# Kernel tuning notes

Measured on AMD Instinct MI355X. Metric: run time of the kernel, lower is better.

Reference implementation:

```python
import jax, jax.numpy as jnp
import numpy as np

B, L, S, N, D, DT, V, H = 32, 256, 5, 1024, 256, 256, 512, 8
Dh = D // H


def layernorm(x, g, b, eps=1e-5):
    m = x.mean(-1, keepdims=True)
    v = ((x - m) ** 2).mean(-1, keepdims=True)
    return (x - m) / jnp.sqrt(v + eps) * g + b


def setup_inputs() -> dict:
    key = jax.random.key(0)
    ks = jax.random.split(key, 16)
    sc = lambda k, shape: jax.random.normal(k, shape, jnp.float32) * 0.02
    return {
        'vis_tokens': jax.random.normal(ks[0], (B, N, D), jnp.float32),
        'left_ctx_ids': jax.random.randint(ks[1], (B, L, S), 0, V),
        'right_ctx_ids': jax.random.randint(ks[2], (B, L, S), 0, V),
        'tgt_ids': jax.random.randint(ks[3], (B, L), 0, V),
        'tgt_mask': jnp.ones((B, L), jnp.float32),
        'vis_mask': jax.random.uniform(ks[4], (B, L, N), jnp.float32),
        'emb_w': sc(ks[5], (V, DT)),          # tied embedding / classifier weight
        'dir_left': sc(ks[6], (DT,)),
        'dir_right': sc(ks[7], (DT,)),
        'txt_proj_w': sc(ks[8], (D, DT)), 'txt_proj_b': jnp.zeros((D,), jnp.float32),
        'q_gamma': jnp.ones((D,), jnp.float32), 'q_beta': jnp.zeros((D,), jnp.float32),
        'k_w': sc(ks[9], (D, D)), 'k_b': jnp.zeros((D,), jnp.float32),
        'v_w': sc(ks[10], (D, D)), 'v_b': jnp.zeros((D,), jnp.float32),
        'kv_gamma': jnp.ones((D,), jnp.float32), 'kv_beta': jnp.zeros((D,), jnp.float32),
        'tau': jnp.asarray(1.0, jnp.float32),
        'cls_b': jnp.zeros((V,), jnp.float32),
        'conv_w_l': sc(ks[11], (DT, DT, 3)),   # fresh random conv weight per call in torch
        'conv_w_r': sc(ks[12], (DT, DT, 3)),
    }


def _ctx_to_query(ctx_ids, dir_tok, conv_w, emb_w, txt_proj_w, txt_proj_b, qg, qb):
    E = emb_w[ctx_ids]                                    # [B,L,S,DT]
    q = jnp.transpose(E, (0, 1, 3, 2)).reshape(B * L, DT, S)
    q = jax.lax.conv_general_dilated(q, conv_w, (1,), [(1, 1)],
                                     dimension_numbers=('NCH', 'OIH', 'NCH'))  # [B*L,DT,S]
    # faithful to torch: flat reinterpretation [B*L,DT,S] -> [B,L,S,DT], then mean over dim 2
    q = q.reshape(B, L, -1, DT).mean(2)                   # [B,L,DT]
    q = q + dir_tok
    return layernorm(q @ txt_proj_w.T + txt_proj_b, qg, qb)  # [B,L,D]


def _cross_attend(Q, Fv, vis_mask, k_w, k_b, v_w, v_b, kvg, kvb, tau):
    K = layernorm(Fv @ k_w.T + k_b, kvg, kvb)             # [B,N,D]
    Vv = layernorm(Fv @ v_w.T + v_b, kvg, kvb)
    q = Q.reshape(B, L, H, Dh).transpose(0, 2, 1, 3)      # [B,H,L,Dh]
    k = K.reshape(B, N, H, Dh).transpose(0, 2, 1, 3)
    v = Vv.reshape(B, N, H, Dh).transpose(0, 2, 1, 3)
    tau_c = jnp.clip(tau, 0.25, 4.0)
    scores = jnp.einsum('bhld,bhnd->bhln', q, k) / (Dh ** 0.5 * tau_c)
    scores = scores * vis_mask[:, None]                   # multiplicative mask
    attn = jax.nn.softmax(scores, axis=-1)                # dropout = identity (eval)
    out = jnp.einsum('bhln,bhnd->bhld', attn, v)
    return out.transpose(0, 2, 1, 3).reshape(B, L, D)


def reference(vis_tokens, left_ctx_ids, right_ctx_ids, tgt_ids, tgt_mask, vis_mask,
              emb_w, dir_left, dir_right, txt_proj_w, txt_proj_b, q_gamma, q_beta,
              k_w, k_b, v_w, v_b, kv_gamma, kv_beta, tau, cls_b, conv_w_l, conv_w_r):
    Ql = _ctx_to_query(left_ctx_ids, dir_left, conv_w_l, emb_w, txt_proj_w, txt_proj_b, q_gamma, q_beta)
    Qr = _ctx_to_query(right_ctx_ids, dir_right, conv_w_r, emb_w, txt_proj_w, txt_proj_b, q_gamma, q_beta)
    Fl = _cross_attend(Ql, vis_tokens, vis_mask, k_w, k_b, v_w, v_b, kv_gamma, kv_beta, tau)
    Fr = _cross_attend(Qr, vis_tokens, vis_mask, k_w, k_b, v_w, v_b, kv_gamma, kv_beta, tau)
    logits_l = Fl @ emb_w.T + cls_b                       # tied classifier
    logits_r = Fr @ emb_w.T + cls_b
    p_l = jax.nn.softmax(logits_l / 2.0, axis=-1)
    p_r = jax.nn.softmax(logits_r / 2.0, axis=-1)
    agree = ((p_l[:, :-1, :] - p_r[:, 1:, :]) ** 2).sum(-1)
    denom = jnp.maximum(tgt_mask[:, :-1].sum(), 1.0)
    loss_sgm = 0.1 * (agree * tgt_mask[:, :-1]).sum() / denom
    return loss_sgm, logits_l, logits_r
```

## Files before the change

kernel.cpp:

```cpp
#include <hip/hip_runtime.h>

typedef __attribute__((ext_vector_type(8))) short short8;
typedef __attribute__((ext_vector_type(4))) short short4v;
typedef __attribute__((ext_vector_type(4))) float f32x4;

__device__ __forceinline__ short f2bf(float x) {
    union { float f; unsigned u; } c; c.f = x;
    unsigned u = c.u;
    u += 0x7fffu + ((u >> 16) & 1u);
    return (short)(u >> 16);
}

__global__ __launch_bounds__(256) void cvt_bf16(const float* __restrict__ s, short* __restrict__ d, int n4) {
    int i = blockIdx.x * 256 + threadIdx.x;
    if (i < n4) {
        float4 v = ((const float4*)s)[i];
        short4 o;
        o.x = f2bf(v.x); o.y = f2bf(v.y); o.z = f2bf(v.z); o.w = f2bf(v.w);
        ((short4*)d)[i] = o;
    }
}

__global__ __launch_bounds__(256) void cvt3(const float* __restrict__ emb, const float* __restrict__ kw,
                                            const float* __restrict__ vw,
                                            short* __restrict__ de, short* __restrict__ dk, short* __restrict__ dv) {
    int i = blockIdx.x * 256 + threadIdx.x;
    const float* s; short* d; int off;
    if (i < 32768) { s = emb; d = de; off = i; }
    else if (i < 49152) { s = kw; d = dk; off = i - 32768; }
    else { s = vw; d = dv; off = i - 49152; }
    float4 v = ((const float4*)s)[off];
    short4 o;
    o.x = f2bf(v.x); o.y = f2bf(v.y); o.z = f2bf(v.z); o.w = f2bf(v.w);
    ((short4*)d)[off] = o;
}

__global__ void build_wfold(const float* __restrict__ cl, const float* __restrict__ cr,
                            float* __restrict__ wfT) {
    const float* conv_w = blockIdx.y ? cr : cl;
    float* o = wfT + (long)blockIdx.y * 327680;
    const int j = blockIdx.x;
    const int ci = threadIdx.x;
    float acc[5] = {0.f, 0.f, 0.f, 0.f, 0.f};
#pragma unroll
    for (int i = 0; i < 5; ++i) {
        int flat = i * 256 + j;
        int c = flat / 5;
        int s = flat % 5;
#pragma unroll
        for (int k = 0; k < 3; ++k) {
            int si = s + k - 1;
            if (si >= 0 && si < 5) acc[si] += conv_w[(c * 256 + ci) * 3 + k];
        }
    }
#pragma unroll
    for (int si = 0; si < 5; ++si)
        o[(si * 256 + ci) * 256 + j] = acc[si] * 0.2f;
}

template <bool BIAS>
__global__ __launch_bounds__(256) void gemm64(const float* __restrict__ A,
                                              const float* __restrict__ W,
                                              const float* __restrict__ bias,
                                              float* __restrict__ C,
                                              int K, int ldC,
                                              long sliceA, long sliceW, long sliceC) {
    A += (long)blockIdx.z * sliceA;
    W += (long)blockIdx.z * sliceW;
    C += (long)blockIdx.z * sliceC;
    const int row0 = blockIdx.x * 64;
    const int col0 = blockIdx.y * 64;
    __shared__ float As[32][68];
    __shared__ float Ws[32][68];
    const int t = threadIdx.x;
    const int tx = t & 15;
    const int ty = t >> 4;
    float acc[4][4] = {};
    for (int kk = 0; kk < K; kk += 32) {
#pragma unroll
        for (int e = 0; e < 8; ++e) {
            int f = t + 256 * e;
            int r = f >> 5, kc = f & 31;
            As[kc][r] = A[(long)(row0 + r) * K + kk + kc];
            Ws[kc][r] = W[(long)(col0 + r) * K + kk + kc];
        }
        __syncthreads();
#pragma unroll
        for (int kc = 0; kc < 32; ++kc) {
            float4 a4 = *(const float4*)&As[kc][ty * 4];
            float4 w4 = *(const float4*)&Ws[kc][tx * 4];
            float av[4] = {a4.x, a4.y, a4.z, a4.w};
            float wv[4] = {w4.x, w4.y, w4.z, w4.w};
#pragma unroll
            for (int i = 0; i < 4; ++i)
#pragma unroll
                for (int jj = 0; jj < 4; ++jj)
                    acc[i][jj] += av[i] * wv[jj];
        }
        __syncthreads();
    }
#pragma unroll
    for (int r = 0; r < 4; ++r) {
        int row = row0 + ty * 4 + r;
#pragma unroll
        for (int c = 0; c < 4; ++c) {
            int col = col0 + tx * 4 + c;
            float v = acc[r][c];
            if (BIAS) v += bias[col];
            C[(long)row * ldC + col] = v;
        }
    }
}

__global__ __launch_bounds__(256) void gemm_bf(const short* __restrict__ A,
                                               const short* __restrict__ W,
                                               const float* __restrict__ bias,
                                               float* __restrict__ Cf,
                                               int K, int ldC,
                                               long sliceA, long sliceC) {
    A += (long)blockIdx.z * sliceA;
    const int row0 = blockIdx.x * 64, col0 = blockIdx.y * 64;
    __shared__ short As[64 * 40];
    __shared__ short Ws[64 * 40];
    const int t = threadIdx.x;
    const int wid = t >> 6, lane = t & 63, sub = lane & 15, quad = lane >> 4;
    const int wy = wid >> 1, wx = wid & 1;
    const int srow = t >> 2, sseg = t & 3;
    f32x4 acc00 = {0.f, 0.f, 0.f, 0.f}, acc01 = acc00, acc10 = acc00, acc11 = acc00;
    for (int kk = 0; kk < K; kk += 32) {
        *(short8*)&As[srow * 40 + sseg * 8] = *(const short8*)&A[(long)(row0 + srow) * K + kk + sseg * 8];
        *(short8*)&Ws[srow * 40 + sseg * 8] = *(const short8*)&W[(long)(col0 + srow) * K + kk + sseg * 8];
        __syncthreads();
        short8 a0 = *(const short8*)&As[(wy * 32 + sub) * 40 + quad * 8];
        short8 a1 = *(const short8*)&As[(wy * 32 + 16 + sub) * 40 + quad * 8];
        short8 b0 = *(const short8*)&Ws[(wx * 32 + sub) * 40 + quad * 8];
        short8 b1 = *(const short8*)&Ws[(wx * 32 + 16 + sub) * 40 + quad * 8];
        acc00 = __builtin_amdgcn_mfma_f32_16x16x32_bf16(a0, b0, acc00, 0, 0, 0);
        acc01 = __builtin_amdgcn_mfma_f32_16x16x32_bf16(a0, b1, acc01, 0, 0, 0);
        acc10 = __builtin_amdgcn_mfma_f32_16x16x32_bf16(a1, b0, acc10, 0, 0, 0);
        acc11 = __builtin_amdgcn_mfma_f32_16x16x32_bf16(a1, b1, acc11, 0, 0, 0);
        __syncthreads();
    }
    Cf += (long)blockIdx.z * sliceC;
#pragma unroll
    for (int i = 0; i < 2; ++i)
#pragma unroll
        for (int j = 0; j < 2; ++j) {
            f32x4 a = (i == 0) ? (j == 0 ? acc00 : acc01) : (j == 0 ? acc10 : acc11);
#pragma unroll
            for (int r = 0; r < 4; ++r) {
                int row = row0 + wy * 32 + i * 16 + quad * 4 + r;
                int col = col0 + wx * 32 + j * 16 + sub;
                Cf[(long)row * ldC + col] = a[r] + bias[col];
            }
        }
}

__global__ __launch_bounds__(256) void gemm_ln(const short* __restrict__ A,
                                               const short* __restrict__ kwbf, const short* __restrict__ vwbf,
                                               const float* __restrict__ k_b, const float* __restrict__ v_b,
                                               const float* __restrict__ gamma, const float* __restrict__ beta,
                                               short* __restrict__ Kout, short* __restrict__ Vt) {
    const bool isV = blockIdx.y != 0;
    const short* W = isV ? vwbf : kwbf;
    const float* bias = isV ? v_b : k_b;
    const int row0 = blockIdx.x * 64;
    __shared__ short As[64 * 40];
    __shared__ short Ws[256 * 40];
    __shared__ float s_mu[64 * 4];
    __shared__ float s_sq[64 * 4];
    __shared__ float s_mv[64 * 2];
    const int t = threadIdx.x;
    const int wid = t >> 6, lane = t & 63, sub = lane & 15, quad = lane >> 4;
    f32x4 acc[4][4];
#pragma unroll
    for (int mi = 0; mi < 4; ++mi)
#pragma unroll
        for (int ni = 0; ni < 4; ++ni) acc[mi][ni] = (f32x4){0.f, 0.f, 0.f, 0.f};

    const int sr = t >> 2, sseg = t & 3;
    for (int kk = 0; kk < 256; kk += 32) {
        *(short8*)&As[sr * 40 + sseg * 8] = *(const short8*)&A[(long)(row0 + sr) * 256 + kk + sseg * 8];
#pragma unroll
        for (int i = 0; i < 4; ++i) {
            int r = i * 64 + sr;
            *(short8*)&Ws[r * 40 + sseg * 8] = *(const short8*)&W[(long)r * 256 + kk + sseg * 8];
        }
        __syncthreads();
        short8 a[4], b[4];
#pragma unroll
        for (int mi = 0; mi < 4; ++mi) a[mi] = *(const short8*)&As[(mi * 16 + sub) * 40 + quad * 8];
#pragma unroll
        for (int ni = 0; ni < 4; ++ni) b[ni] = *(const short8*)&Ws[(wid * 64 + ni * 16 + sub) * 40 + quad * 8];
#pragma unroll
        for (int mi = 0; mi < 4; ++mi)
#pragma unroll
            for (int ni = 0; ni < 4; ++ni)
                acc[mi][ni] = __builtin_amdgcn_mfma_f32_16x16x32_bf16(a[mi], b[ni], acc[mi][ni], 0, 0, 0);
        __syncthreads();
    }
#pragma unroll
    for (int ni = 0; ni < 4; ++ni) {
        float bv = bias[wid * 64 + ni * 16 + sub];
#pragma unroll
        for (int mi = 0; mi < 4; ++mi)
#pragma unroll
            for (int r = 0; r < 4; ++r) acc[mi][ni][r] += bv;
    }
#pragma unroll
    for (int mi = 0; mi < 4; ++mi) {
#pragma unroll
        for (int r = 0; r < 4; ++r) {
            float s = 0.f, q2 = 0.f;
#pragma unroll
            for (int ni = 0; ni < 4; ++ni) {
                float v = acc[mi][ni][r];
                s += v; q2 += v * v;
            }
#pragma unroll
            for (int off = 8; off; off >>= 1) {
                s += __shfl_xor(s, off, 16);
                q2 += __shfl_xor(q2, off, 16);
            }
            if (sub == 0) {
                int row = mi * 16 + quad * 4 + r;
                s_mu[row * 4 + wid] = s;
                s_sq[row * 4 + wid] = q2;
            }
        }
    }
    __syncthreads();
    if (t < 64) {
        float s = s_mu[t * 4] + s_mu[t * 4 + 1] + s_mu[t * 4 + 2] + s_mu[t * 4 + 3];
        float q2 = s_sq[t * 4] + s_sq[t * 4 + 1] + s_sq[t * 4 + 2] + s_sq[t * 4 + 3];
        float mean = s * (1.0f / 256.0f);
        float var = q2 * (1.0f / 256.0f) - mean * mean;
        s_mv[t * 2] = mean;
        s_mv[t * 2 + 1] = rsqrtf(var + 1e-5f);
    }
    __syncthreads();
#pragma unroll
    for (int ni = 0; ni < 4; ++ni) {
        int col = wid * 64 + ni * 16 + sub;
        float g = gamma[col], bb = beta[col];
        if (!isV) {
#pragma unroll
            for (int mi = 0; mi < 4; ++mi)
#pragma unroll
                for (int r = 0; r < 4; ++r) {
                    int row = mi * 16 + quad * 4 + r;
                    float v = (acc[mi][ni][r] - s_mv[row * 2]) * s_mv[row * 2 + 1] * g + bb;
                    Kout[(long)(row0 + row) * 256 + col] = f2bf(v);
                }
        } else {
            int h = col >> 5, dh = col & 31;
#pragma unroll
            for (int mi = 0; mi < 4; ++mi) {
                int rowb = row0 + mi * 16 + quad * 4;
                short4 o;
#pragma unroll
                for (int r = 0; r < 4; ++r) {
                    int row = mi * 16 + quad * 4 + r;
                    float v = (acc[mi][ni][r] - s_mv[row * 2]) * s_mv[row * 2 + 1] * g + bb;
                    ((short*)&o)[r] = f2bf(v);
                }
                int gb = rowb >> 10, n = rowb & 1023;
                *(short4*)&Vt[((long)(gb * 8 + h) * 32 + dh) * 1024 + n] = o;
            }
        }
    }
}

__global__ void bias_dir_kernel(const float* __restrict__ tp, const float* __restrict__ tpb,
                                const float* __restrict__ dirL, const float* __restrict__ dirR,
                                float* __restrict__ biasL, float* __restrict__ biasR) {
    const float* dir = blockIdx.x ? dirR : dirL;
    float* outp = blockIdx.x ? biasR : biasL;
    __shared__ float sdir[256];
    const int d = threadIdx.x;
    sdir[d] = dir[d];
    __syncthreads();
    float acc = tpb[d];
    for (int j = 0; j < 256; ++j) acc += tp[d * 256 + j] * sdir[j];
    outp[d] = acc;
}

__global__ __launch_bounds__(256) void q_build(const int* __restrict__ idsL, const int* __restrict__ idsR,
                                               const float* __restrict__ Pp,
                                               const float* __restrict__ biasL, const float* __restrict__ biasR,
                                               const float* __restrict__ qg, const float* __restrict__ qb,
                                               short* __restrict__ Qbf) {
    const int wid = threadIdx.x >> 6, lane = threadIdx.x & 63;
    const int bl = blockIdx.x * 4 + wid;
    const bool right = blockIdx.y != 0;
    const int* ids = right ? idsR : idsL;
    const float* P = right ? Pp + 655360 : Pp;
    const float* bias = right ? biasR : biasL;
    const int d0 = lane * 4;
    float4 acc = *(const float4*)&bias[d0];
#pragma unroll
    for (int s = 0; s < 5; ++s) {
        int tok = ids[bl * 5 + s];
        float4 p = *(const float4*)&P[(long)(s * 512 + tok) * 256 + d0];
        acc.x += p.x; acc.y += p.y; acc.z += p.z; acc.w += p.w;
    }
    float sum = acc.x + acc.y + acc.z + acc.w;
    float sq = acc.x * acc.x + acc.y * acc.y + acc.z * acc.z + acc.w * acc.w;
#pragma unroll
    for (int off = 32; off; off >>= 1) {
        sum += __shfl_xor(sum, off, 64);
        sq += __shfl_xor(sq, off, 64);
    }
    float mean = sum * (1.0f / 256.0f);
    float var = sq * (1.0f / 256.0f) - mean * mean;
    float rstd = rsqrtf(var + 1e-5f);
    float4 g = *(const float4*)&qg[d0];
    float4 bb = *(const float4*)&qb[d0];
    short4 o;
    o.x = f2bf((acc.x - mean) * rstd * g.x + bb.x);
    o.y = f2bf((acc.y - mean) * rstd * g.y + bb.y);
    o.z = f2bf((acc.z - mean) * rstd * g.z + bb.z);
    o.w = f2bf((acc.w - mean) * rstd * g.w + bb.w);
    *(short4*)&Qbf[(right ? 2097152L : 0L) + (long)bl * 256 + d0] = o;
}

__device__ __forceinline__ void proc_chunk(
    short8 ak0, short8 ak1, short4v v00, short4v v01, short4v v10, short4v v11,
    const float* mlds, int sub, int quad, float inv2,
    const short8 (&bqL)[4], const short8 (&bqR)[4],
    f32x4 (&oL)[4][2], f32x4 (&oR)[4][2], float (&psL)[4], float (&psR)[4]) {
    short8 av0, av1;
#pragma unroll
    for (int j = 0; j < 4; ++j) {
        av0[j] = v00[j]; av0[4 + j] = v01[j];
        av1[j] = v10[j]; av1[4 + j] = v11[j];
    }
    const int sw = (quad ^ (sub & 7)) << 2;
#pragma unroll
    for (int lt = 0; lt < 4; ++lt) {
        const int mi = ((lt * 16 + sub) << 5) + sw;
        float4 mk0 = *(const float4*)&mlds[mi];
        float4 mk1 = *(const float4*)&mlds[mi ^ 16];
        float m0x = mk0.x * inv2, m0y = mk0.y * inv2, m0z = mk0.z * inv2, m0w = mk0.w * inv2;
        float m1x = mk1.x * inv2, m1y = mk1.y * inv2, m1z = mk1.z * inv2, m1w = mk1.w * inv2;
        {
            f32x4 c0 = {0.f, 0.f, 0.f, 0.f}, c1 = c0;
            c0 = __builtin_amdgcn_mfma_f32_16x16x32_bf16(ak0, bqL[lt], c0, 0, 0, 0);
            c1 = __builtin_amdgcn_mfma_f32_16x16x32_bf16(ak1, bqL[lt], c1, 0, 0, 0);
            float p0 = __builtin_amdgcn_exp2f(c0[0] * m0x);
            float p1 = __builtin_amdgcn_exp2f(c0[1] * m0y);
            float p2 = __builtin_amdgcn_exp2f(c0[2] * m0z);
            float p3 = __builtin_amdgcn_exp2f(c0[3] * m0w);
            float p4 = __builtin_amdgcn_exp2f(c1[0] * m1x);
            float p5 = __builtin_amdgcn_exp2f(c1[1] * m1y);
            float p6 = __builtin_amdgcn_exp2f(c1[2] * m1z);
            float p7 = __builtin_amdgcn_exp2f(c1[3] * m1w);
            psL[lt] += ((p0 + p1) + (p2 + p3)) + ((p4 + p5) + (p6 + p7));
            short8 p8;
            p8[0] = f2bf(p0); p8[1] = f2bf(p1); p8[2] = f2bf(p2); p8[3] = f2bf(p3);
            p8[4] = f2bf(p4); p8[5] = f2bf(p5); p8[6] = f2bf(p6); p8[7] = f2bf(p7);
            oL[lt][0] = __builtin_amdgcn_mfma_f32_16x16x32_bf16(av0, p8, oL[lt][0], 0, 0, 0);
            oL[lt][1] = __builtin_amdgcn_mfma_f32_16x16x32_bf16(av1, p8, oL[lt][1], 0, 0, 0);
        }
        {
            f32x4 c0 = {0.f, 0.f, 0.f, 0.f}, c1 = c0;
            c0 = __builtin_amdgcn_mfma_f32_16x16x32_bf16(ak0, bqR[lt], c0, 0, 0, 0);
            c1 = __builtin_amdgcn_mfma_f32_16x16x32_bf16(ak1, bqR[lt], c1, 0, 0, 0);
            float p0 = __builtin_amdgcn_exp2f(c0[0] * m0x);
            float p1 = __builtin_amdgcn_exp2f(c0[1] * m0y);
            float p2 = __builtin_amdgcn_exp2f(c0[2] * m0z);
            float p3 = __builtin_amdgcn_exp2f(c0[3] * m0w);
            float p4 = __builtin_amdgcn_exp2f(c1[0] * m1x);
            float p5 = __builtin_amdgcn_exp2f(c1[1] * m1y);
            float p6 = __builtin_amdgcn_exp2f(c1[2] * m1z);
            float p7 = __builtin_amdgcn_exp2f(c1[3] * m1w);
            psR[lt] += ((p0 + p1) + (p2 + p3)) + ((p4 + p5) + (p6 + p7));
            short8 p8;
            p8[0] = f2bf(p0); p8[1] = f2bf(p1); p8[2] = f2bf(p2); p8[3] = f2bf(p3);
            p8[4] = f2bf(p4); p8[5] = f2bf(p5); p8[6] = f2bf(p6); p8[7] = f2bf(p7);
            oR[lt][0] = __builtin_amdgcn_mfma_f32_16x16x32_bf16(av0, p8, oR[lt][0], 0, 0, 0);
            oR[lt][1] = __builtin_amdgcn_mfma_f32_16x16x32_bf16(av1, p8, oR[lt][1], 0, 0, 0);
        }
    }
}

__global__ __launch_bounds__(512, 1) void attn_wave(const short* __restrict__ Qbf,
                                                    const short* __restrict__ Kbf,
                                                    const short* __restrict__ Vt,
                                                    const float* __restrict__ vis_mask,
                                                    const float* __restrict__ tau_p,
                                                    short* __restrict__ Fbf) {
    const int t = threadIdx.x;
    const int wid = t >> 6, lane = t & 63, sub = lane & 15, quad = lane >> 4;
    const int gb = ((blockIdx.x & 7) << 5) | (blockIdx.x >> 3);
    const int b = gb >> 3;
    const int lb = (gb >> 1) & 3;
    const int hq = gb & 1;
    const int wh = wid >> 1, nh = wid & 1;
    const int h = hq * 4 + wh;
    const int l0 = lb * 64;
    float tau = fminf(fmaxf(tau_p[0], 0.25f), 4.0f);
    const float inv2 = 1.4426950408889634f / (5.656854249492381f * tau);

    __shared__ float mbuf[2 * 4096];
    __shared__ float red[4][64][72];

    const int s0 = t * 2;
    const int l_s = (s0 >> 3) & 63, nh_s = s0 >> 9;
    const int n4a = s0 & 7, n4b = n4a + 1;
    const float* mrow0 = vis_mask + (long)(b * 256 + l0 + l_s) * 1024 + nh_s * 512 + 4 * (n4a ^ (l_s & 7));
    const float* mrow1 = vis_mask + (long)(b * 256 + l0 + l_s) * 1024 + nh_s * 512 + 4 * (n4b ^ (l_s & 7));
    float* mdst0 = mbuf + nh_s * 2048 + l_s * 32 + n4a * 4;
    float* mdst1 = mbuf + nh_s * 2048 + l_s * 32 + n4b * 4;

    short8 bqL[4], bqR[4];
#pragma unroll
    for (int lt = 0; lt < 4; ++lt) {
        const long qoff = (long)(b * 256 + l0 + lt * 16 + sub) * 256 + h * 32 + quad * 8;
        bqL[lt] = *(const short8*)&Qbf[qoff];
        bqR[lt] = *(const short8*)&Qbf[2097152 + qoff];
    }

    const short* Kb = Kbf + (long)b * 262144 + h * 32;
    const short* Vb = Vt + (long)(b * 8 + h) * 32768;
    const float* mld = mbuf + nh * 2048;

    f32x4 oL[4][2], oR[4][2];
    float psL[4], psR[4];
#pragma unroll
    for (int lt = 0; lt < 4; ++lt) {
        oL[lt][0] = (f32x4){0.f, 0.f, 0.f, 0.f}; oL[lt][1] = oL[lt][0];
        oR[lt][0] = oL[lt][0]; oR[lt][1] = oL[lt][0];
        psL[lt] = 0.f; psR[lt] = 0.f;
    }

    const int nbeg = nh << 9;

#define LOADK(A0, A1, N)                                                      \
    A0 = *(const short8*)&Kb[(long)((N) + sub) * 256 + quad * 8];             \
    A1 = *(const short8*)&Kb[(long)((N) + 16 + sub) * 256 + quad * 8];
#define LOADV(W00, W01, W10, W11, N)                                          \
    W00 = *(const short4v*)&Vb[(long)sub * 1024 + (N) + quad * 4];            \
    W01 = *(const short4v*)&Vb[(long)sub * 1024 + (N) + 16 + quad * 4];       \
    W10 = *(const short4v*)&Vb[(long)(16 + sub) * 1024 + (N) + quad * 4];     \
    W11 = *(const short4v*)&Vb[(long)(16 + sub) * 1024 + (N) + 16 + quad * 4];

    short8 ak0A, ak1A, ak0B, ak1B;
    short4v v00A, v01A, v10A, v11A, v00B, v01B, v10B, v11B;
    float4 mr0, mr1;

    mr0 = *(const float4*)&mrow0[0];
    mr1 = *(const float4*)&mrow1[0];
    *(float4*)&mdst0[0] = mr0;
    *(float4*)&mdst1[0] = mr1;
    LOADK(ak0A, ak1A, nbeg)
    LOADV(v00A, v01A, v10A, v11A, nbeg)
    __syncthreads();

#pragma unroll 1
    for (int j = 0; j < 8; ++j) {
        const int n0 = nbeg + j * 64;
        LOADK(ak0B, ak1B, n0 + 32)
        LOADV(v00B, v01B, v10B, v11B, n0 + 32)
        {
            const int nrel = j * 64 + 32;
            mr0 = *(const float4*)&mrow0[nrel];
            mr1 = *(const float4*)&mrow1[nrel];
        }
        proc_chunk(ak0A, ak1A, v00A, v01A, v10A, v11A, mld, sub, quad, inv2,
                   bqL, bqR, oL, oR, psL, psR);
        *(float4*)&mdst0[4096] = mr0;
        *(float4*)&mdst1[4096] = mr1;
        __syncthreads();
        const int nx = (j < 7) ? n0 + 64 : nbeg;
        LOADK(ak0A, ak1A, nx)
        LOADV(v00A, v01A, v10A, v11A, nx)
        {
            const int nrel = (j < 7) ? j * 64 + 64 : 0;
            mr0 = *(const float4*)&mrow0[nrel];
            mr1 = *(const float4*)&mrow1[nrel];
        }
        proc_chunk(ak0B, ak1B, v00B, v01B, v10B, v11B, mld + 4096, sub, quad, inv2,
                   bqL, bqR, oL, oR, psL, psR);
        *(float4*)&mdst0[0] = mr0;
        *(float4*)&mdst1[0] = mr1;
        __syncthreads();
    }
#undef LOADK
#undef LOADV

#pragma unroll
    for (int lt = 0; lt < 4; ++lt) {
        psL[lt] += __shfl_xor(psL[lt], 16, 64); psL[lt] += __shfl_xor(psL[lt], 32, 64);
        psR[lt] += __shfl_xor(psR[lt], 16, 64); psR[lt] += __shfl_xor(psR[lt], 32, 64);
    }

    if (nh == 1) {
        float* p = &red[wh][lane][0];
#pragma unroll
        for (int lt = 0; lt < 4; ++lt) {
            *(f32x4*)(p + lt * 8) = oL[lt][0];
            *(f32x4*)(p + lt * 8 + 4) = oL[lt][1];
            *(f32x4*)(p + 32 + lt * 8) = oR[lt][0];
            *(f32x4*)(p + 32 + lt * 8 + 4) = oR[lt][1];
            p[64 + lt] = psL[lt];
            p[68 + lt] = psR[lt];
        }
    }
    __syncthreads();
    if (nh == 1) return;
    {
        const float* p = &red[wh][lane][0];
#pragma unroll
        for (int lt = 0; lt < 4; ++lt) {
            f32x4 e0 = *(const f32x4*)(p + lt * 8);
            f32x4 e1 = *(const f32x4*)(p + lt * 8 + 4);
            f32x4 e2 = *(const f32x4*)(p + 32 + lt * 8);
            f32x4 e3 = *(const f32x4*)(p + 32 + lt * 8 + 4);
#pragma unroll
            for (int r = 0; r < 4; ++r) {
                oL[lt][0][r] += e0[r]; oL[lt][1][r] += e1[r];
                oR[lt][0][r] += e2[r]; oR[lt][1][r] += e3[r];
            }
            psL[lt] += p[64 + lt];
            psR[lt] += p[68 + lt];
        }
    }

#pragma unroll
    for (int lt = 0; lt < 4; ++lt) {
        const long fo = (long)(b * 256 + l0 + lt * 16 + sub) * 256 + h * 32 + quad * 4;
        const float rL = 1.0f / psL[lt], rR = 1.0f / psR[lt];
        short4v s0v, s1v;
#pragma unroll
        for (int r = 0; r < 4; ++r) { s0v[r] = f2bf(oL[lt][0][r] * rL); s1v[r] = f2bf(oL[lt][1][r] * rL); }
        *(short4v*)&Fbf[fo] = s0v;
        *(short4v*)&Fbf[fo + 16] = s1v;
#pragma unroll
        for (int r = 0; r < 4; ++r) { s0v[r] = f2bf(oR[lt][0][r] * rR); s1v[r] = f2bf(oR[lt][1][r] * rR); }
        *(short4v*)&Fbf[2097152 + fo] = s0v;
        *(short4v*)&Fbf[2097152 + fo + 16] = s1v;
    }
}

__global__ __launch_bounds__(256) void loss_pair(const float* __restrict__ logits,
                                                 const float* __restrict__ tgt_mask,
                                                 float* __restrict__ partials) {
    const int wid = threadIdx.x >> 6, lane = threadIdx.x & 63;
    const int pid = blockIdx.x * 4 + wid;
    const int b = pid / 255, l = pid - b * 255;
    const float* ll = logits + (long)(b * 256 + l) * 512;
    const float* lr = logits + 4194304 + (long)(b * 256 + l + 1) * 512;
    float a[8], c[8];
#pragma unroll
    for (int j = 0; j < 8; ++j) {
        a[j] = ll[lane + 64 * j] * 0.5f;
        c[j] = lr[lane + 64 * j] * 0.5f;
    }
    float ml = -1e30f, mr = -1e30f;
#pragma unroll
    for (int j = 0; j < 8; ++j) { ml = fmaxf(ml, a[j]); mr = fmaxf(mr, c[j]); }
#pragma unroll
    for (int off = 32; off; off >>= 1) {
        ml = fmaxf(ml, __shfl_xor(ml, off, 64));
        mr = fmaxf(mr, __shfl_xor(mr, off, 64));
    }
    float sl = 0.f, sr = 0.f;
#pragma unroll
    for (int j = 0; j < 8; ++j) {
        a[j] = __expf(a[j] - ml); sl += a[j];
        c[j] = __expf(c[j] - mr); sr += c[j];
    }
#pragma unroll
    for (int off = 32; off; off >>= 1) {
        sl += __shfl_xor(sl, off, 64);
        sr += __shfl_xor(sr, off, 64);
    }
    float rl = 1.0f / sl, rr = 1.0f / sr;
    float sq = 0.f;
#pragma unroll
    for (int j = 0; j < 8; ++j) {
        float d = a[j] * rl - c[j] * rr;
        sq += d * d;
    }
#pragma unroll
    for (int off = 32; off; off >>= 1) sq += __shfl_xor(sq, off, 64);

    __shared__ float sred[4];
    if (lane == 0) sred[wid] = sq * tgt_mask[b * 256 + l];
    __syncthreads();
    if (threadIdx.x == 0)
        partials[blockIdx.x] = (sred[0] + sred[1]) + (sred[2] + sred[3]);
}

__global__ __launch_bounds__(256) void loss_final(const float* __restrict__ tgt_mask,
                                                  const float* __restrict__ partials,
                                                  float* __restrict__ outp) {
    const int t = threadIdx.x;
    float s = 0.f, acc = 0.f;
    for (int i = t; i < 32 * 255; i += 256) {
        int b = i / 255, l = i % 255;
        s += tgt_mask[b * 256 + l];
    }
    for (int i = t; i < 2040; i += 256) acc += partials[i];
    __shared__ float red[256];
    __shared__ float reda[256];
    red[t] = s;
    reda[t] = acc;
    __syncthreads();
    for (int st = 128; st; st >>= 1) {
        if (t < st) { red[t] += red[t + st]; reda[t] += reda[t + st]; }
        __syncthreads();
    }
    if (t == 0) outp[0] = 0.1f * reda[0] / fmaxf(red[0], 1.0f);
}

extern "C" void kernel_launch(void* const* d_in, const int* in_sizes, int n_in,
                              void* d_out, int out_size, void* d_ws, size_t ws_size,
                              hipStream_t stream) {
    const float* vis_tokens = (const float*)d_in[0];
    const int* idsL = (const int*)d_in[1];
    const int* idsR = (const int*)d_in[2];
    const float* tgt_mask = (const float*)d_in[4];
    const float* vis_mask = (const float*)d_in[5];
    const float* emb_w = (const float*)d_in[6];
    const float* dirL = (const float*)d_in[7];
    const float* dirR = (const float*)d_in[8];
    const float* tp_w = (const float*)d_in[9];
    const float* tp_b = (const float*)d_in[10];
    const float* q_g = (const float*)d_in[11];
    const float* q_b = (const float*)d_in[12];
    const float* k_w = (const float*)d_in[13];
    const float* k_b = (const float*)d_in[14];
    const float* v_w = (const float*)d_in[15];
    const float* v_b = (const float*)d_in[16];
    const float* kv_g = (const float*)d_in[17];
    const float* kv_b = (const float*)d_in[18];
    const float* tau = (const float*)d_in[19];
    const float* cls_b = (const float*)d_in[20];
    const float* conv_l = (const float*)d_in[21];
    const float* conv_r = (const float*)d_in[22];
    float* out = (float*)d_out;

    short* sws = (short*)d_ws;
    short* visbf = sws;
    short* embbf = visbf + 8388608;
    short* kwbf  = embbf + 131072;
    short* vwbf  = kwbf + 65536;
    short* Kbf   = vwbf + 65536;
    short* Vt    = Kbf + 8388608;
    short* Qbf   = Vt + 8388608;
    short* Fbf   = Qbf + 4194304;
    float* wfT   = (float*)(Fbf + 4194304);
    float* Ms    = wfT + 655360;
    float* Pp    = Ms + 655360;
    float* bias_l = Pp + 1310720;
    float* bias_r = bias_l + 256;
    float* partials = bias_r + 256;

    cvt_bf16<<<8192, 256, 0, stream>>>(vis_tokens, visbf, 2097152);
    cvt3<<<256, 256, 0, stream>>>(emb_w, k_w, v_w, embbf, kwbf, vwbf);

    build_wfold<<<dim3(256, 2), 256, 0, stream>>>(conv_l, conv_r, wfT);
    gemm64<false><<<dim3(4, 4, 10), 256, 0, stream>>>(tp_w, wfT, nullptr, Ms, 256, 256, 0, 65536, 65536);
    gemm64<false><<<dim3(8, 4, 10), 256, 0, stream>>>(emb_w, Ms, nullptr, Pp, 256, 256, 0, 65536, 131072);
    bias_dir_kernel<<<2, 256, 0, stream>>>(tp_w, tp_b, dirL, dirR, bias_l, bias_r);
    q_build<<<dim3(2048, 2), 256, 0, stream>>>(idsL, idsR, Pp, bias_l, bias_r, q_g, q_b, Qbf);

    gemm_ln<<<dim3(512, 2), 256, 0, stream>>>(visbf, kwbf, vwbf, k_b, v_b, kv_g, kv_b, Kbf, Vt);

    attn_wave<<<256, 512, 0, stream>>>(Qbf, Kbf, Vt, vis_mask, tau, Fbf);

    gemm_bf<<<dim3(128, 8, 2), 256, 0, stream>>>(Fbf, embbf, cls_b, out + 1, 256, 512,
                                                 2097152, 4194304);

    loss_pair<<<2040, 256, 0, stream>>>(out + 1, tgt_mask, partials);
    loss_final<<<1, 256, 0, stream>>>(tgt_mask, partials, out);
}
```

Before: 334.5 us.

## Split attention key range across four waves per head with 1024-thread blocks

The attention kernel doubles its block to 1024 threads, so each head's 1024 visual tokens are split across four waves instead of two. Each wave now runs four loop iterations instead of eight, and the per-wave partial results are combined in three serialized shared-memory reduction rounds. Other changes: the mask is pre-scaled by the softmax constant when staged into LDS, the bf16 conversion uses packed hardware intrinsics, and K/V are loaded just before use rather than software-prefetched a chunk ahead. The intent is more waves per CU to hide latency. The costs are extra reduction rounds and barriers, and load latency is no longer hidden by the explicit prefetch.

```diff
diff --git a/kernel.cpp b/kernel.cpp
--- a/kernel.cpp
+++ b/kernel.cpp
@@ -1,4 +1,5 @@
 #include <hip/hip_runtime.h>
+#include <hip/hip_bf16.h>
 
 typedef __attribute__((ext_vector_type(8))) short short8;
 typedef __attribute__((ext_vector_type(4))) short short4v;
@@ -9,6 +10,12 @@
     unsigned u = c.u;
     u += 0x7fffu + ((u >> 16) & 1u);
     return (short)(u >> 16);
+}
+
+__device__ __forceinline__ unsigned pk2(float a, float b) {
+    union { __hip_bfloat162 h2; unsigned u; } cv;
+    cv.h2 = __float22bfloat162_rn(float2{a, b});
+    return cv.u;
 }
 
 __global__ __launch_bounds__(256) void cvt_bf16(const float* __restrict__ s, short* __restrict__ d, int n4) {
@@ -326,7 +333,7 @@
 
 __device__ __forceinline__ void proc_chunk(
     short8 ak0, short8 ak1, short4v v00, short4v v01, short4v v10, short4v v11,
-    const float* mlds, int sub, int quad, float inv2,
+    const float* mlds, int sub, int quad,
     const short8 (&bqL)[4], const short8 (&bqR)[4],
     f32x4 (&oL)[4][2], f32x4 (&oR)[4][2], float (&psL)[4], float (&psR)[4]) {
     short8 av0, av1;
@@ -341,77 +348,75 @@
         const int mi = ((lt * 16 + sub) << 5) + sw;
         float4 mk0 = *(const float4*)&mlds[mi];
         float4 mk1 = *(const float4*)&mlds[mi ^ 16];
-        float m0x = mk0.x * inv2, m0y = mk0.y * inv2, m0z = mk0.z * inv2, m0w = mk0.w * inv2;
-        float m1x = mk1.x * inv2, m1y = mk1.y * inv2, m1z = mk1.z * inv2, m1w = mk1.w * inv2;
         {
             f32x4 c0 = {0.f, 0.f, 0.f, 0.f}, c1 = c0;
             c0 = __builtin_amdgcn_mfma_f32_16x16x32_bf16(ak0, bqL[lt], c0, 0, 0, 0);
             c1 = __builtin_amdgcn_mfma_f32_16x16x32_bf16(ak1, bqL[lt], c1, 0, 0, 0);
-            float p0 = __builtin_amdgcn_exp2f(c0[0] * m0x);
-            float p1 = __builtin_amdgcn_exp2f(c0[1] * m0y);
-            float p2 = __builtin_amdgcn_exp2f(c0[2] * m0z);
-            float p3 = __builtin_amdgcn_exp2f(c0[3] * m0w);
-            float p4 = __builtin_amdgcn_exp2f(c1[0] * m1x);
-            float p5 = __builtin_amdgcn_exp2f(c1[1] * m1y);
-            float p6 = __builtin_amdgcn_exp2f(c1[2] * m1z);
-            float p7 = __builtin_amdgcn_exp2f(c1[3] * m1w);
+            float p0 = __builtin_amdgcn_exp2f(c0[0] * mk0.x);
+            float p1 = __builtin_amdgcn_exp2f(c0[1] * mk0.y);
+            float p2 = __builtin_amdgcn_exp2f(c0[2] * mk0.z);
+            float p3 = __builtin_amdgcn_exp2f(c0[3] * mk0.w);
+            float p4 = __builtin_amdgcn_exp2f(c1[0] * mk1.x);
+            float p5 = __builtin_amdgcn_exp2f(c1[1] * mk1.y);
+            float p6 = __builtin_amdgcn_exp2f(c1[2] * mk1.z);
+            float p7 = __builtin_amdgcn_exp2f(c1[3] * mk1.w);
             psL[lt] += ((p0 + p1) + (p2 + p3)) + ((p4 + p5) + (p6 + p7));
-            short8 p8;
-            p8[0] = f2bf(p0); p8[1] = f2bf(p1); p8[2] = f2bf(p2); p8[3] = f2bf(p3);
-            p8[4] = f2bf(p4); p8[5] = f2bf(p5); p8[6] = f2bf(p6); p8[7] = f2bf(p7);
-            oL[lt][0] = __builtin_amdgcn_mfma_f32_16x16x32_bf16(av0, p8, oL[lt][0], 0, 0, 0);
-            oL[lt][1] = __builtin_amdgcn_mfma_f32_16x16x32_bf16(av1, p8, oL[lt][1], 0, 0, 0);
+            union { short8 s; unsigned u[4]; } pp;
+            pp.u[0] = pk2(p0, p1); pp.u[1] = pk2(p2, p3);
+            pp.u[2] = pk2(p4, p5); pp.u[3] = pk2(p6, p7);
+            oL[lt][0] = __builtin_amdgcn_mfma_f32_16x16x32_bf16(av0, pp.s, oL[lt][0], 0, 0, 0);
+            oL[lt][1] = __builtin_amdgcn_mfma_f32_16x16x32_bf16(av1, pp.s, oL[lt][1], 0, 0, 0);
         }
         {
             f32x4 c0 = {0.f, 0.f, 0.f, 0.f}, c1 = c0;
             c0 = __builtin_amdgcn_mfma_f32_16x16x32_bf16(ak0, bqR[lt], c0, 0, 0, 0);
             c1 = __builtin_amdgcn_mfma_f32_16x16x32_bf16(ak1, bqR[lt], c1, 0, 0, 0);
-            float p0 = __builtin_amdgcn_exp2f(c0[0] * m0x);
-            float p1 = __builtin_amdgcn_exp2f(c0[1] * m0y);
-            float p2 = __builtin_amdgcn_exp2f(c0[2] * m0z);
-            float p3 = __builtin_amdgcn_exp2f(c0[3] * m0w);
-            float p4 = __builtin_amdgcn_exp2f(c1[0] * m1x);
-            float p5 = __builtin_amdgcn_exp2f(c1[1] * m1y);
-            float p6 = __builtin_amdgcn_exp2f(c1[2] * m1z);
-            float p7 = __builtin_amdgcn_exp2f(c1[3] * m1w);
+            float p0 = __builtin_amdgcn_exp2f(c0[0] * mk0.x);
+            float p1 = __builtin_amdgcn_exp2f(c0[1] * mk0.y);
+            float p2 = __builtin_amdgcn_exp2f(c0[2] * mk0.z);
+            float p3 = __builtin_amdgcn_exp2f(c0[3] * mk0.w);
+            float p4 = __builtin_amdgcn_exp2f(c1[0] * mk1.x);
+            float p5 = __builtin_amdgcn_exp2f(c1[1] * mk1.y);
+            float p6 = __builtin_amdgcn_exp2f(c1[2] * mk1.z);
+            float p7 = __builtin_amdgcn_exp2f(c1[3] * mk1.w);
             psR[lt] += ((p0 + p1) + (p2 + p3)) + ((p4 + p5) + (p6 + p7));
-            short8 p8;
-            p8[0] = f2bf(p0); p8[1] = f2bf(p1); p8[2] = f2bf(p2); p8[3] = f2bf(p3);
-            p8[4] = f2bf(p4); p8[5] = f2bf(p5); p8[6] = f2bf(p6); p8[7] = f2bf(p7);
-            oR[lt][0] = __builtin_amdgcn_mfma_f32_16x16x32_bf16(av0, p8, oR[lt][0], 0, 0, 0);
-            oR[lt][1] = __builtin_amdgcn_mfma_f32_16x16x32_bf16(av1, p8, oR[lt][1], 0, 0, 0);
-        }
-    }
-}
-
-__global__ __launch_bounds__(512, 1) void attn_wave(const short* __restrict__ Qbf,
-                                                    const short* __restrict__ Kbf,
-                                                    const short* __restrict__ Vt,
-                                                    const float* __restrict__ vis_mask,
-                                                    const float* __restrict__ tau_p,
-                                                    short* __restrict__ Fbf) {
+            union { short8 s; unsigned u[4]; } pp;
+            pp.u[0] = pk2(p0, p1); pp.u[1] = pk2(p2, p3);
+            pp.u[2] = pk2(p4, p5); pp.u[3] = pk2(p6, p7);
+            oR[lt][0] = __builtin_amdgcn_mfma_f32_16x16x32_bf16(av0, pp.s, oR[lt][0], 0, 0, 0);
+            oR[lt][1] = __builtin_amdgcn_mfma_f32_16x16x32_bf16(av1, pp.s, oR[lt][1], 0, 0, 0);
+        }
+    }
+}
+
+__global__ __launch_bounds__(1024, 1) void attn_wave(const short* __restrict__ Qbf,
+                                                     const short* __restrict__ Kbf,
+                                                     const short* __restrict__ Vt,
+                                                     const float* __restrict__ vis_mask,
+                                                     const float* __restrict__ tau_p,
+                                                     short* __restrict__ Fbf) {
     const int t = threadIdx.x;
     const int wid = t >> 6, lane = t & 63, sub = lane & 15, quad = lane >> 4;
     const int gb = ((blockIdx.x & 7) << 5) | (blockIdx.x >> 3);
     const int b = gb >> 3;
     const int lb = (gb >> 1) & 3;
     const int hq = gb & 1;
-    const int wh = wid >> 1, nh = wid & 1;
+    const int wh = wid >> 2, nh = wid & 3;
     const int h = hq * 4 + wh;
     const int l0 = lb * 64;
     float tau = fminf(fmaxf(tau_p[0], 0.25f), 4.0f);
     const float inv2 = 1.4426950408889634f / (5.656854249492381f * tau);
 
-    __shared__ float mbuf[2 * 4096];
-    __shared__ float red[4][64][72];
+    __shared__ float smem[19456];
 
     const int s0 = t * 2;
-    const int l_s = (s0 >> 3) & 63, nh_s = s0 >> 9;
-    const int n4a = s0 & 7, n4b = n4a + 1;
-    const float* mrow0 = vis_mask + (long)(b * 256 + l0 + l_s) * 1024 + nh_s * 512 + 4 * (n4a ^ (l_s & 7));
-    const float* mrow1 = vis_mask + (long)(b * 256 + l0 + l_s) * 1024 + nh_s * 512 + 4 * (n4b ^ (l_s & 7));
-    float* mdst0 = mbuf + nh_s * 2048 + l_s * 32 + n4a * 4;
-    float* mdst1 = mbuf + nh_s * 2048 + l_s * 32 + n4b * 4;
+    const int nh_s = s0 >> 9;
+    const int l_s = (s0 >> 3) & 63;
+    const int n4a = s0 & 7, n4b = n4a | 1;
+    const float* mrow0 = vis_mask + (long)(b * 256 + l0 + l_s) * 1024 + nh_s * 256 + n4a * 4;
+    const float* mrow1 = vis_mask + (long)(b * 256 + l0 + l_s) * 1024 + nh_s * 256 + n4b * 4;
+    float* md0 = smem + nh_s * 2048 + l_s * 32 + ((n4a ^ (l_s & 7)) << 2);
+    float* md1 = smem + nh_s * 2048 + l_s * 32 + ((n4b ^ (l_s & 7)) << 2);
 
     short8 bqL[4], bqR[4];
 #pragma unroll
@@ -423,7 +428,8 @@
 
     const short* Kb = Kbf + (long)b * 262144 + h * 32;
     const short* Vb = Vt + (long)(b * 8 + h) * 32768;
-    const float* mld = mbuf + nh * 2048;
+    const float* mld0 = smem + nh * 2048;
+    const float* mld1 = smem + 8192 + nh * 2048;
 
     f32x4 oL[4][2], oR[4][2];
     float psL[4], psR[4];
@@ -434,7 +440,7 @@
         psL[lt] = 0.f; psR[lt] = 0.f;
     }
 
-    const int nbeg = nh << 9;
+    const int nbeg = nh << 8;
 
 #define LOADK(A0, A1, N)                                                      \
     A0 = *(const short8*)&Kb[(long)((N) + sub) * 256 + quad * 8];             \
@@ -445,45 +451,47 @@
     W10 = *(const short4v*)&Vb[(long)(16 + sub) * 1024 + (N) + quad * 4];     \
     W11 = *(const short4v*)&Vb[(long)(16 + sub) * 1024 + (N) + 16 + quad * 4];
 
-    short8 ak0A, ak1A, ak0B, ak1B;
-    short4v v00A, v01A, v10A, v11A, v00B, v01B, v10B, v11B;
-    float4 mr0, mr1;
-
-    mr0 = *(const float4*)&mrow0[0];
-    mr1 = *(const float4*)&mrow1[0];
-    *(float4*)&mdst0[0] = mr0;
-    *(float4*)&mdst1[0] = mr1;
-    LOADK(ak0A, ak1A, nbeg)
-    LOADV(v00A, v01A, v10A, v11A, nbeg)
+    {
+        float4 a0 = *(const float4*)&mrow0[0];
+        float4 a1 = *(const float4*)&mrow1[0];
+        a0.x *= inv2; a0.y *= inv2; a0.z *= inv2; a0.w *= inv2;
+        a1.x *= inv2; a1.y *= inv2; a1.z *= inv2; a1.w *= inv2;
+        *(float4*)md0 = a0;
+        *(float4*)md1 = a1;
+    }
     __syncthreads();
 
 #pragma unroll 1
-    for (int j = 0; j < 8; ++j) {
+    for (int j = 0; j < 4; ++j) {
         const int n0 = nbeg + j * 64;
-        LOADK(ak0B, ak1B, n0 + 32)
-        LOADV(v00B, v01B, v10B, v11B, n0 + 32)
+        float4 ma0 = *(const float4*)&mrow0[j * 64 + 32];
+        float4 ma1 = *(const float4*)&mrow1[j * 64 + 32];
+        ma0.x *= inv2; ma0.y *= inv2; ma0.z *= inv2; ma0.w *= inv2;
+        ma1.x *= inv2; ma1.y *= inv2; ma1.z *= inv2; ma1.w *= inv2;
         {
-            const int nrel = j * 64 + 32;
-            mr0 = *(const float4*)&mrow0[nrel];
-            mr1 = *(const float4*)&mrow1[nrel];
-        }
-        proc_chunk(ak0A, ak1A, v00A, v01A, v10A, v11A, mld, sub, quad, inv2,
-                   bqL, bqR, oL, oR, psL, psR);
-        *(float4*)&mdst0[4096] = mr0;
-        *(float4*)&mdst1[4096] = mr1;
-        __syncthreads();
-        const int nx = (j < 7) ? n0 + 64 : nbeg;
-        LOADK(ak0A, ak1A, nx)
-        LOADV(v00A, v01A, v10A, v11A, nx)
+            short8 ak0, ak1; short4v v00, v01, v10, v11;
+            LOADK(ak0, ak1, n0)
+            LOADV(v00, v01, v10, v11, n0)
+            proc_chunk(ak0, ak1, v00, v01, v10, v11, mld0, sub, quad,
+                       bqL, bqR, oL, oR, psL, psR);
+        }
+        *(float4*)(md0 + 8192) = ma0;
+        *(float4*)(md1 + 8192) = ma1;
+        __syncthreads();
+        const int nrel = (j < 3) ? j * 64 + 64 : 0;
+        float4 mb0 = *(const float4*)&mrow0[nrel];
+        float4 mb1 = *(const float4*)&mrow1[nrel];
+        mb0.x *= inv2; mb0.y *= inv2; mb0.z *= inv2; mb0.w *= inv2;
+        mb1.x *= inv2; mb1.y *= inv2; mb1.z *= inv2; mb1.w *= inv2;
         {
-            const int nrel = (j < 7) ? j * 64 + 64 : 0;
-            mr0 = *(const float4*)&mrow0[nrel];
-            mr1 = *(const float4*)&mrow1[nrel];
-        }
-        proc_chunk(ak0B, ak1B, v00B, v01B, v10B, v11B, mld + 4096, sub, quad, inv2,
-                   bqL, bqR, oL, oR, psL, psR);
-        *(float4*)&mdst0[0] = mr0;
-        *(float4*)&mdst1[0] = mr1;
+            short8 ak0, ak1; short4v v00, v01, v10, v11;
+            LOADK(ak0, ak1, n0 + 32)
+            LOADV(v00, v01, v10, v11, n0 + 32)
+            proc_chunk(ak0, ak1, v00, v01, v10, v11, mld1, sub, quad,
+                       bqL, bqR, oL, oR, psL, psR);
+        }
+        *(float4*)md0 = mb0;
+        *(float4*)md1 = mb1;
         __syncthreads();
     }
 #undef LOADK
@@ -495,37 +503,41 @@
         psR[lt] += __shfl_xor(psR[lt], 16, 64); psR[lt] += __shfl_xor(psR[lt], 32, 64);
     }
 
-    if (nh == 1) {
-        float* p = &red[wh][lane][0];
-#pragma unroll
-        for (int lt = 0; lt < 4; ++lt) {
-            *(f32x4*)(p + lt * 8) = oL[lt][0];
-            *(f32x4*)(p + lt * 8 + 4) = oL[lt][1];
-            *(f32x4*)(p + 32 + lt * 8) = oR[lt][0];
-            *(f32x4*)(p + 32 + lt * 8 + 4) = oR[lt][1];
-            p[64 + lt] = psL[lt];
-            p[68 + lt] = psR[lt];
-        }
-    }
-    __syncthreads();
-    if (nh == 1) return;
-    {
-        const float* p = &red[wh][lane][0];
-#pragma unroll
-        for (int lt = 0; lt < 4; ++lt) {
-            f32x4 e0 = *(const f32x4*)(p + lt * 8);
-            f32x4 e1 = *(const f32x4*)(p + lt * 8 + 4);
-            f32x4 e2 = *(const f32x4*)(p + 32 + lt * 8);
-            f32x4 e3 = *(const f32x4*)(p + 32 + lt * 8 + 4);
-#pragma unroll
-            for (int r = 0; r < 4; ++r) {
-                oL[lt][0][r] += e0[r]; oL[lt][1][r] += e1[r];
-                oR[lt][0][r] += e2[r]; oR[lt][1][r] += e3[r];
+#pragma unroll 1
+    for (int r = 1; r <= 3; ++r) {
+        if (nh == r) {
+            float* p = smem + (wh * 64 + lane) * 76;
+#pragma unroll
+            for (int lt = 0; lt < 4; ++lt) {
+                *(f32x4*)(p + lt * 8) = oL[lt][0];
+                *(f32x4*)(p + lt * 8 + 4) = oL[lt][1];
+                *(f32x4*)(p + 32 + lt * 8) = oR[lt][0];
+                *(f32x4*)(p + 32 + lt * 8 + 4) = oR[lt][1];
+                p[64 + lt] = psL[lt];
+                p[68 + lt] = psR[lt];
             }
-            psL[lt] += p[64 + lt];
-            psR[lt] += p[68 + lt];
-        }
-    }
+        }
+        __syncthreads();
+        if (nh == 0) {
+            const float* p = smem + (wh * 64 + lane) * 76;
+#pragma unroll
+            for (int lt = 0; lt < 4; ++lt) {
+                f32x4 e0 = *(const f32x4*)(p + lt * 8);
+                f32x4 e1 = *(const f32x4*)(p + lt * 8 + 4);
+                f32x4 e2 = *(const f32x4*)(p + 32 + lt * 8);
+                f32x4 e3 = *(const f32x4*)(p + 32 + lt * 8 + 4);
+#pragma unroll
+                for (int q = 0; q < 4; ++q) {
+                    oL[lt][0][q] += e0[q]; oL[lt][1][q] += e1[q];
+                    oR[lt][0][q] += e2[q]; oR[lt][1][q] += e3[q];
+                }
+                psL[lt] += p[64 + lt];
+                psR[lt] += p[68 + lt];
+            }
+        }
+        __syncthreads();
+    }
+    if (nh != 0) return;
 
 #pragma unroll
     for (int lt = 0; lt < 4; ++lt) {
@@ -669,7 +681,7 @@
 
     gemm_ln<<<dim3(512, 2), 256, 0, stream>>>(visbf, kwbf, vwbf, k_b, v_b, kv_g, kv_b, Kbf, Vt);
 
-    attn_wave<<<256, 512, 0, stream>>>(Qbf, Kbf, Vt, vis_mask, tau, Fbf);
+    attn_wave<<<256, 1024, 0, stream>>>(Qbf, Kbf, Vt, vis_mask, tau, Fbf);
 
     gemm_bf<<<dim3(128, 8, 2), 256, 0, stream>>>(Fbf, embbf, cls_b, out + 1, 256, 512,
                                                  2097152, 4194304);
```

After: 547.0 us. +63.5%, slower.
